# Kernel tuning notes

Hardware: AMD Instinct MI355X
Metric: run time of the kernel (lower is better)

The kernel has to match this reference:

```python
import jax, jax.numpy as jnp
import numpy as np
from jax import lax

B, C, T, L, H = 8, 32, 9, 512, 8
D = C // H  # head_dim = 4


def _l2norm(y):
    # torch F.normalize(dim=-1): x / max(||x||_2, 1e-12)
    n = jnp.sqrt(jnp.sum(y * y, axis=-1, keepdims=True))
    return y / jnp.maximum(n, 1e-12)


def setup_inputs() -> dict:
    key = jax.random.key(0)
    ks = jax.random.split(key, 12)
    def w(i, shape, s=0.05):
        return jax.random.normal(ks[i], shape, jnp.float32) * s
    return {
        "x": jax.random.normal(ks[0], (B, C, T, L), jnp.float32),
        "Wq": w(1, (C, C)), "bq": jnp.zeros((C,), jnp.float32),
        "Wk": w(2, (C, C)), "bk": jnp.zeros((C,), jnp.float32),
        "Wv": w(3, (C, C)), "bv": jnp.zeros((C,), jnp.float32),
        "Wm": w(4, (C, C)), "bm": jnp.zeros((C,), jnp.float32),
        "W_logit": jnp.eye(H, dtype=jnp.float32) + w(5, (H, H), 0.02),
        "W_ctx": jnp.eye(H, dtype=jnp.float32) + w(6, (H, H), 0.02),
        "rel_pos_bias": w(7, (H, 2 * L - 1), 0.02),
        "pre_prompt": w(8, (1, C, 1, L), 0.02),
        "conv_w": w(9, (C, C, T, 1)), "conv_b": jnp.zeros((C,), jnp.float32),
        "bn_g": jnp.ones((C,), jnp.float32), "bn_b": jnp.zeros((C,), jnp.float32),
        "pl_w": w(10, (L, L)), "pl_b": jnp.zeros((L,), jnp.float32),
        "atten_flag": 1,
    }


def _forward(x, Wq, bq, Wk, bk, Wv, bv, Wm, bm, W_logit, W_ctx,
             rel_pos_bias, pre_prompt, conv_w, conv_b, bn_g, bn_b, pl_w, pl_b):
    b = x.shape[0]
    xi = jnp.transpose(x, (0, 2, 3, 1))  # (b, t, l, c)

    def proj(W, bb):
        y = (xi @ W.T + bb).reshape(b, T, L, H, D).transpose(0, 1, 3, 2, 4)  # (b,t,h,l,d)
        return _l2norm(y)

    q = proj(Wq, bq)
    k = proj(Wk, bk)
    v = proj(Wv, bv)

    logits = jnp.einsum('bthid,bthjd->bthij', q, k) / jnp.float32(np.sqrt(D))
    idx = jnp.arange(L)
    rel = jnp.clip(idx[:, None] - idx[None, :] + (L - 1), 0, 2 * L - 2)  # (l,l)
    logits = logits + rel_pos_bias[:, rel][None, None]  # (h,l,l) broadcast over b,t
    logits = jnp.einsum('bthij,hH->btHij', logits, W_logit)
    atten = jax.nn.softmax(logits, axis=-1)
    atten = jnp.einsum('bthij,hH->btHij', atten, W_ctx)
    x_att = jnp.einsum('bthij,bthjd->bthid', atten, v)
    x_att = x_att.transpose(0, 1, 3, 2, 4).reshape(b, T, L, C)
    x_att = (x_att @ Wm.T + bm).transpose(0, 3, 1, 2)  # (b, c, t, l)

    pp = jnp.broadcast_to(pre_prompt, (b, C, 1, L))
    con = jnp.concatenate([x_att[:, :, :T - 1], pp], axis=2)  # (b, c, T, l)
    y = lax.conv_general_dilated(con, conv_w, (1, 1), 'VALID',
                                 dimension_numbers=('NCHW', 'OIHW', 'NCHW'))
    y = y + conv_b[None, :, None, None]  # (b, c, 1, l)
    # BatchNorm2d in eval with running stats (mean=0, var=1), eps=1e-5
    y = y / jnp.sqrt(jnp.float32(1.0 + 1e-5))
    y = jax.nn.relu(y * bn_g[None, :, None, None] + bn_b[None, :, None, None])
    p = y @ pl_w.T + pl_b  # Linear over last dim (token_len)
    p = x_att[:, :, T - 1:] - p
    return jnp.concatenate([x_att[:, :, :T - 1], p], axis=2)


def reference(x, Wq, bq, Wk, bk, Wv, bv, Wm, bm, W_logit, W_ctx,
              rel_pos_bias, pre_prompt, conv_w, conv_b, bn_g, bn_b,
              pl_w, pl_b, atten_flag):
    # atten_flag is accepted but unused, matching the original module
    return _forward(x, Wq, bq, Wk, bk, Wv, bv, Wm, bm, W_logit, W_ctx,
                    rel_pos_bias, pre_prompt, conv_w, conv_b, bn_g, bn_b, pl_w, pl_b)
```

## Files before the change

kernel.cpp:

```cpp
#include <hip/hip_runtime.h>
#include <math.h>

#define BB 8
#define CC 32
#define TT 9
#define LL 512
#define HH 8
#define DD 4
#define NBT (BB*TT)
#define RELN (2*LL-1)
#define RLN2 1.4426950408889634f

typedef float  f4v __attribute__((ext_vector_type(4)));
typedef int    i4v __attribute__((ext_vector_type(4)));
typedef short  s8v __attribute__((ext_vector_type(8)));

#define EXP2(x) __builtin_amdgcn_exp2f(x)

__device__ __forceinline__ unsigned cvtpk(float lo, float hi) {
  unsigned u;
  asm("v_cvt_pk_bf16_f32 %0, %1, %2" : "=v"(u) : "v"(lo), "v"(hi));
  return u;
}

__global__ __launch_bounds__(256) void prep_kernel(
    const float* __restrict__ plw, float* __restrict__ plwT,
    const float* __restrict__ rpb, const float* __restrict__ Wl,
    float* __restrict__ mbr) {
  if (blockIdx.x < 256) {
    __shared__ float tile[32][33];
    int bx = (blockIdx.x & 15) * 32, by = (blockIdx.x >> 4) * 32;
    int tx = threadIdx.x & 31, ty = threadIdx.x >> 5;
    #pragma unroll
    for (int yy = ty; yy < 32; yy += 8)
      tile[yy][tx] = plw[(by + yy)*LL + bx + tx];
    __syncthreads();
    #pragma unroll
    for (int yy = ty; yy < 32; yy += 8)
      plwT[(bx + yy)*LL + by + tx] = tile[tx][yy];
  } else {
    int x = (blockIdx.x - 256) * 256 + threadIdx.x;
    if (x >= RELN) return;
    int idx = 1022 - x;
    float r[HH];
    #pragma unroll
    for (int h = 0; h < HH; ++h) r[h] = rpb[h*RELN + idx];
    #pragma unroll
    for (int Ho = 0; Ho < HH; ++Ho) {
      float acc = 0.f;
      #pragma unroll
      for (int h = 0; h < HH; ++h) acc += r[h] * Wl[h*HH + Ho];
      mbr[Ho*1024 + x] = RLN2 * acc;
    }
  }
}

__global__ __launch_bounds__(256) void proj_kernel(
    const float* __restrict__ x,
    const float* __restrict__ Wq, const float* __restrict__ bq,
    const float* __restrict__ Wk, const float* __restrict__ bk,
    const float* __restrict__ Wv, const float* __restrict__ bv,
    float* __restrict__ qo, short* __restrict__ kbo, short* __restrict__ vt) {
  int gidx = blockIdx.x * 256 + threadIdx.x;
  int l  = gidx & (LL-1);
  int bt = gidx >> 9;
  int b = bt / TT, t = bt - b*TT;
  const int hq = blockIdx.y * 2;

  float xv[CC];
  #pragma unroll
  for (int c = 0; c < CC; ++c)
    xv[c] = x[((b*CC + c)*TT + t)*LL + l];

  #pragma unroll
  for (int h = hq; h < hq + 2; ++h) {
    float yv[DD];
    #pragma unroll
    for (int d = 0; d < DD; ++d) {
      int co = h*DD + d;
      float acc = bq[co];
      #pragma unroll
      for (int ci = 0; ci < CC; ++ci) acc += xv[ci] * Wq[co*CC + ci];
      yv[d] = acc;
    }
    float n = sqrtf(yv[0]*yv[0] + yv[1]*yv[1] + yv[2]*yv[2] + yv[3]*yv[3]);
    float inv = 0.5f * RLN2 / fmaxf(n, 1e-12f);
    *reinterpret_cast<float4*>(&qo[((size_t)bt*LL + l)*CC + h*DD]) =
        make_float4(yv[0]*inv, yv[1]*inv, yv[2]*inv, yv[3]*inv);
  }
  {
    unsigned ku[4];
    #pragma unroll
    for (int hh = 0; hh < 2; ++hh) {
      int h = hq + hh;
      float yv[DD];
      #pragma unroll
      for (int d = 0; d < DD; ++d) {
        int co = h*DD + d;
        float acc = bk[co];
        #pragma unroll
        for (int ci = 0; ci < CC; ++ci) acc += xv[ci] * Wk[co*CC + ci];
        yv[d] = acc;
      }
      float n = sqrtf(yv[0]*yv[0] + yv[1]*yv[1] + yv[2]*yv[2] + yv[3]*yv[3]);
      float inv = 1.0f / fmaxf(n, 1e-12f);
      ku[hh*2]   = cvtpk(yv[0]*inv, yv[1]*inv);
      ku[hh*2+1] = cvtpk(yv[2]*inv, yv[3]*inv);
    }
    *reinterpret_cast<uint4*>(kbo + ((size_t)bt*LL + l)*CC + hq*DD) =
        make_uint4(ku[0], ku[1], ku[2], ku[3]);
  }
  #pragma unroll
  for (int h = hq; h < hq + 2; ++h) {
    float yv[DD];
    #pragma unroll
    for (int d = 0; d < DD; ++d) {
      int co = h*DD + d;
      float acc = bv[co];
      #pragma unroll
      for (int ci = 0; ci < CC; ++ci) acc += xv[ci] * Wv[co*CC + ci];
      yv[d] = acc;
    }
    float n = sqrtf(yv[0]*yv[0] + yv[1]*yv[1] + yv[2]*yv[2] + yv[3]*yv[3]);
    float inv = 1.0f / fmaxf(n, 1e-12f);
    #pragma unroll
    for (int d = 0; d < DD; ++d) {
      unsigned u = cvtpk(yv[d]*inv, yv[d]*inv);
      int co = h*DD + d;
      reinterpret_cast<unsigned short*>(vt)[((size_t)bt*CC + co)*LL + l] =
          (unsigned short)(u & 0xffffu);
    }
  }
}

__global__ __launch_bounds__(256, 2) void attn_kernel(
    const float* __restrict__ q, const short* __restrict__ kb,
    const short* __restrict__ vt,
    const float* __restrict__ Wl, const float* __restrict__ Wc,
    const float* __restrict__ mbr,
    const float* __restrict__ Wm, const float* __restrict__ bm,
    float* __restrict__ out, float* __restrict__ xm8) {
  __shared__ float xch[2][64][9];
  __shared__ float xt[32][33];
  __shared__ float sWm[32][33];
  __shared__ float sbm[32];

  const int wgid = blockIdx.x;
  const int id   = (wgid & 7) * 144 + (wgid >> 3);
  const int bt   = id >> 4;
  const int iblk = id & 15;
  const int b    = bt / TT, t = bt - b*TT;

  const int tid  = threadIdx.x;
  const int w    = __builtin_amdgcn_readfirstlane(tid >> 6);
  const int lane = tid & 63;
  const int g    = lane >> 4;
  const int c16  = lane & 15;
  const int it   = iblk*32 + (w & 1)*16;
  const int Hb   = (w >> 1)*4;

  {
    int c4 = tid * 4;
    int co = c4 >> 5, ci = c4 & 31;
    float4 wv = *reinterpret_cast<const float4*>(Wm + co*CC + ci);
    sWm[co][ci] = wv.x; sWm[co][ci+1] = wv.y; sWm[co][ci+2] = wv.z; sWm[co][ci+3] = wv.w;
    if (tid < 32) sbm[tid] = bm[tid];
  }

  s8v bq4[4];
  {
    float qp[8];
    const float* qr = q + ((size_t)bt*LL + it + c16)*CC + g*8;
    float4 qa = *reinterpret_cast<const float4*>(qr);
    float4 qb = *reinterpret_cast<const float4*>(qr + 4);
    qp[0]=qa.x; qp[1]=qa.y; qp[2]=qa.z; qp[3]=qa.w;
    qp[4]=qb.x; qp[5]=qb.y; qp[6]=qb.z; qp[7]=qb.w;
    const int h0 = g*2;
    #pragma unroll
    for (int hh = 0; hh < 4; ++hh) {
      const int H = Hb + hh;
      const float wla = Wl[h0*HH + H];
      const float wlb = Wl[(h0+1)*HH + H];
      i4v uq;
      uq[0] = (int)cvtpk(qp[0]*wla, qp[1]*wla);
      uq[1] = (int)cvtpk(qp[2]*wla, qp[3]*wla);
      uq[2] = (int)cvtpk(qp[4]*wlb, qp[5]*wlb);
      uq[3] = (int)cvtpk(qp[6]*wlb, qp[7]*wlb);
      bq4[hh] = __builtin_bit_cast(s8v, uq);
    }
  }

  const short* kbase = kb + ((size_t)bt*LL)*CC + (size_t)c16*CC + g*8;
  const short* vb0 = vt + ((size_t)bt*CC)*LL + (size_t)c16*LL + 8*g;
  const short* vb1 = vb0 + 16*LL;
  const float* mbase = mbr + Hb*1024 + 511 + 4*g - it - c16;

  f4v t0[4], t1[4];
  float den[4];
  #pragma unroll
  for (int hh = 0; hh < 4; ++hh) {
    t0[hh] = (f4v){0.f,0.f,0.f,0.f};
    t1[hh] = (f4v){0.f,0.f,0.f,0.f};
    den[hh] = 0.f;
  }

  const int s0b = (c16 + 32*(g & 1))*4;
  const int s1b = s0b + 64;
  const bool useA = (g < 2);

  #pragma unroll 1
  for (int jp = 0; jp < 16; ++jp) {
    const int j0 = jp*32;
    s8v ak0 = *reinterpret_cast<const s8v*>(kbase + (size_t)j0*CC);
    s8v ak1 = *reinterpret_cast<const s8v*>(kbase + (size_t)(j0+16)*CC);
    s8v v0  = *reinterpret_cast<const s8v*>(vb0 + j0);
    s8v v1  = *reinterpret_cast<const s8v*>(vb1 + j0);

    #pragma unroll
    for (int hh = 0; hh < 4; ++hh) {
      const float* m = mbase + hh*1024 + j0;
      unsigned uA0, uA1, uB0, uB1;
      {
        f4v cb = { m[0], m[1], m[2], m[3] };
        f4v d = __builtin_amdgcn_mfma_f32_16x16x32_bf16(ak0, bq4[hh], cb, 0, 0, 0);
        float e0 = EXP2(d[0]), e1 = EXP2(d[1]), e2 = EXP2(d[2]), e3 = EXP2(d[3]);
        den[hh] += (e0 + e1) + (e2 + e3);
        uA0 = cvtpk(e0, e1); uA1 = cvtpk(e2, e3);
      }
      {
        f4v cb = { m[16], m[17], m[18], m[19] };
        f4v d = __builtin_amdgcn_mfma_f32_16x16x32_bf16(ak1, bq4[hh], cb, 0, 0, 0);
        float e0 = EXP2(d[0]), e1 = EXP2(d[1]), e2 = EXP2(d[2]), e3 = EXP2(d[3]);
        den[hh] += (e0 + e1) + (e2 + e3);
        uB0 = cvtpk(e0, e1); uB1 = cvtpk(e2, e3);
      }
      int a00 = __builtin_amdgcn_ds_bpermute(s0b, (int)uA0);
      int b00 = __builtin_amdgcn_ds_bpermute(s0b, (int)uB0);
      int a01 = __builtin_amdgcn_ds_bpermute(s0b, (int)uA1);
      int b01 = __builtin_amdgcn_ds_bpermute(s0b, (int)uB1);
      int a10 = __builtin_amdgcn_ds_bpermute(s1b, (int)uA0);
      int b10 = __builtin_amdgcn_ds_bpermute(s1b, (int)uB0);
      int a11 = __builtin_amdgcn_ds_bpermute(s1b, (int)uA1);
      int b11 = __builtin_amdgcn_ds_bpermute(s1b, (int)uB1);
      i4v pv;
      pv[0] = useA ? a00 : b00;
      pv[1] = useA ? a01 : b01;
      pv[2] = useA ? a10 : b10;
      pv[3] = useA ? a11 : b11;
      s8v pa = __builtin_bit_cast(s8v, pv);
      t0[hh] = __builtin_amdgcn_mfma_f32_16x16x32_bf16(pa, v0, t0[hh], 0, 0, 0);
      t1[hh] = __builtin_amdgcn_mfma_f32_16x16x32_bf16(pa, v1, t1[hh], 0, 0, 0);
    }
  }

  f4v fin0 = {0.f,0.f,0.f,0.f}, fin1 = {0.f,0.f,0.f,0.f};
  #pragma unroll
  for (int hh = 0; hh < 4; ++hh) {
    const int H = Hb + hh;
    float dn = den[hh];
    dn += __shfl_xor(dn, 16);
    dn += __shfl_xor(dn, 32);
    float inv = __builtin_amdgcn_rcpf(dn);
    const float wclo = Wc[H*HH + (c16 >> 2)];
    const float wchi = Wc[H*HH + 4 + (c16 >> 2)];
    #pragma unroll
    for (int r = 0; r < 4; ++r) {
      float ir = __int_as_float(
          __builtin_amdgcn_ds_bpermute((4*g + r)*4, __float_as_int(inv)));
      fin0[r] += t0[hh][r] * (ir * wclo);
      fin1[r] += t1[hh][r] * (ir * wchi);
    }
  }

  if (w >= 2) {
    #pragma unroll
    for (int r = 0; r < 4; ++r) {
      xch[w-2][lane][r]     = fin0[r];
      xch[w-2][lane][4 + r] = fin1[r];
    }
  }
  __syncthreads();
  if (w < 2) {
    #pragma unroll
    for (int r = 0; r < 4; ++r) {
      float o0 = fin0[r] + xch[w][lane][r];
      float o1 = fin1[r] + xch[w][lane][4 + r];
      const int row = w*16 + 4*g + r;
      xt[row][c16]      = o0;
      xt[row][16 + c16] = o1;
    }
  }
  __syncthreads();

  {
    const int row = tid & 31;
    const int cos = (tid >> 5) * 4;
    float a0 = sbm[cos], a1 = sbm[cos+1], a2 = sbm[cos+2], a3 = sbm[cos+3];
    #pragma unroll
    for (int c = 0; c < CC; ++c) {
      float xv = xt[row][c];
      a0 += xv * sWm[cos][c];
      a1 += xv * sWm[cos+1][c];
      a2 += xv * sWm[cos+2][c];
      a3 += xv * sWm[cos+3][c];
    }
    const int l = iblk*32 + row;
    float av[4] = {a0, a1, a2, a3};
    #pragma unroll
    for (int u = 0; u < 4; ++u) {
      int co = cos + u;
      if (t < TT-1) out[((b*CC + co)*TT + t)*LL + l] = av[u];
      else          xm8[(b*CC + co)*LL + l] = av[u];
    }
  }
}

__global__ __launch_bounds__(1024) void convpl_kernel(
    const float* __restrict__ out_in, const float* __restrict__ pp,
    const float* __restrict__ cw, const float* __restrict__ cb,
    const float* __restrict__ bng, const float* __restrict__ bnb,
    const float* __restrict__ plwT, const float* __restrict__ plb,
    const float* __restrict__ xm8, float* __restrict__ out) {
  __shared__ float sy[LL];
  __shared__ float part[2][LL];
  int bc = blockIdx.x;
  int b = bc >> 5, co = bc & 31;
  int tid = threadIdx.x;
  int l = tid & (LL-1);
  int h = tid >> 9;

  float acc = (h == 0) ? cb[co] : 0.f;
  #pragma unroll
  for (int cc = 0; cc < 16; ++cc) {
    int ci = h*16 + cc;
    const float* base = out_in + ((b*CC + ci)*TT)*LL + l;
    const float* wv = cw + (co*CC + ci)*TT;
    #pragma unroll
    for (int tq = 0; tq < TT-1; ++tq) acc += base[tq*LL] * wv[tq];
    acc += pp[ci*LL + l] * wv[TT-1];
  }
  part[h][l] = acc;
  __syncthreads();
  if (h == 0) {
    float scale = bng[co] * 0.999995000037499687f;
    sy[l] = fmaxf((part[0][l] + part[1][l]) * scale + bnb[co], 0.f);
  }
  __syncthreads();
  float accp = (h == 0) ? plb[l] : 0.f;
  #pragma unroll 4
  for (int lq = 0; lq < 256; ++lq) {
    int ll = h*256 + lq;
    accp += sy[ll] * plwT[ll*LL + l];
  }
  part[h][l] = accp;
  __syncthreads();
  if (h == 0)
    out[((b*CC + co)*TT + (TT-1))*LL + l] = xm8[bc*LL + l] - (part[0][l] + part[1][l]);
}

extern "C" void kernel_launch(void* const* d_in, const int* in_sizes, int n_in,
                              void* d_out, int out_size, void* d_ws, size_t ws_size,
                              hipStream_t stream) {
  const float* x    = (const float*)d_in[0];
  const float* Wq   = (const float*)d_in[1];
  const float* bq   = (const float*)d_in[2];
  const float* Wk   = (const float*)d_in[3];
  const float* bk   = (const float*)d_in[4];
  const float* Wv   = (const float*)d_in[5];
  const float* bv   = (const float*)d_in[6];
  const float* Wm   = (const float*)d_in[7];
  const float* bm   = (const float*)d_in[8];
  const float* Wl   = (const float*)d_in[9];
  const float* Wc   = (const float*)d_in[10];
  const float* rpb  = (const float*)d_in[11];
  const float* pp   = (const float*)d_in[12];
  const float* cw   = (const float*)d_in[13];
  const float* cb   = (const float*)d_in[14];
  const float* bng  = (const float*)d_in[15];
  const float* bnb  = (const float*)d_in[16];
  const float* plw  = (const float*)d_in[17];
  const float* plb  = (const float*)d_in[18];
  float* out = (float*)d_out;

  float* ws = (float*)d_ws;
  const size_t NE = (size_t)NBT*LL*CC;
  float* q_ws   = ws;
  short* kb_ws  = (short*)(q_ws + NE);
  short* vt_ws  = kb_ws + NE;
  float* xm8    = (float*)(vt_ws + NE);
  float* plwT   = xm8 + (size_t)BB*CC*LL;
  float* mbias  = plwT + (size_t)LL*LL;

  prep_kernel<<<260, 256, 0, stream>>>(plw, plwT, rpb, Wl, mbias);
  proj_kernel<<<dim3(144,4), 256, 0, stream>>>(x, Wq, bq, Wk, bk, Wv, bv,
                                               q_ws, kb_ws, vt_ws);
  attn_kernel<<<NBT*16, 256, 0, stream>>>(q_ws, kb_ws, vt_ws, Wl, Wc, mbias,
                                          Wm, bm, out, xm8);
  convpl_kernel<<<BB*CC, 1024, 0, stream>>>(out, pp, cw, cb, bng, bnb,
                                            plwT, plb, xm8, out);
}
```

Measured before the change: 108.4 us.

## Compute transposed PV product with 16x16x16 MFMA to drop bpermute shuffles

Instead of redistributing the exponentiated scores across lanes with eight ds_bpermute ops per head before a 16x16x32 MFMA, the kernel now feeds the score registers directly as the B operand of 16x16x16 bf16 MFMAs with V as the A operand. This computes the transposed output tile, so V loads become four 4-element loads and the epilogue normalisation and xt store indexing are transposed to match. The aim is to remove LDS-permute traffic and select logic from the inner loop, at the cost of twice as many (smaller) MFMA instructions issued through inline asm.

```diff
diff --git a/kernel.cpp b/kernel.cpp
--- a/kernel.cpp
+++ b/kernel.cpp
@@ -13,9 +13,14 @@
 
 typedef float  f4v __attribute__((ext_vector_type(4)));
 typedef int    i4v __attribute__((ext_vector_type(4)));
+typedef int    i2v __attribute__((ext_vector_type(2)));
 typedef short  s8v __attribute__((ext_vector_type(8)));
+typedef short  s4v __attribute__((ext_vector_type(4)));
 
 #define EXP2(x) __builtin_amdgcn_exp2f(x)
+
+#define MFMA16(acc, a, b) \
+  asm("v_mfma_f32_16x16x16_bf16 %0, %1, %2, %0" : "+v"(acc) : "v"(a), "v"(b))
 
 __device__ __forceinline__ unsigned cvtpk(float lo, float hi) {
   unsigned u;
@@ -191,7 +196,7 @@
   }
 
   const short* kbase = kb + ((size_t)bt*LL)*CC + (size_t)c16*CC + g*8;
-  const short* vb0 = vt + ((size_t)bt*CC)*LL + (size_t)c16*LL + 8*g;
+  const short* vb0 = vt + ((size_t)bt*CC)*LL + (size_t)c16*LL;
   const short* vb1 = vb0 + 16*LL;
   const float* mbase = mbr + Hb*1024 + 511 + 4*g - it - c16;
 
@@ -203,18 +208,16 @@
     t1[hh] = (f4v){0.f,0.f,0.f,0.f};
     den[hh] = 0.f;
   }
-
-  const int s0b = (c16 + 32*(g & 1))*4;
-  const int s1b = s0b + 64;
-  const bool useA = (g < 2);
 
   #pragma unroll 1
   for (int jp = 0; jp < 16; ++jp) {
     const int j0 = jp*32;
     s8v ak0 = *reinterpret_cast<const s8v*>(kbase + (size_t)j0*CC);
     s8v ak1 = *reinterpret_cast<const s8v*>(kbase + (size_t)(j0+16)*CC);
-    s8v v0  = *reinterpret_cast<const s8v*>(vb0 + j0);
-    s8v v1  = *reinterpret_cast<const s8v*>(vb1 + j0);
+    s4v va00 = *reinterpret_cast<const s4v*>(vb0 + j0 + 4*g);
+    s4v va01 = *reinterpret_cast<const s4v*>(vb0 + j0 + 16 + 4*g);
+    s4v va10 = *reinterpret_cast<const s4v*>(vb1 + j0 + 4*g);
+    s4v va11 = *reinterpret_cast<const s4v*>(vb1 + j0 + 16 + 4*g);
 
     #pragma unroll
     for (int hh = 0; hh < 4; ++hh) {
@@ -224,32 +227,22 @@
         f4v cb = { m[0], m[1], m[2], m[3] };
         f4v d = __builtin_amdgcn_mfma_f32_16x16x32_bf16(ak0, bq4[hh], cb, 0, 0, 0);
         float e0 = EXP2(d[0]), e1 = EXP2(d[1]), e2 = EXP2(d[2]), e3 = EXP2(d[3]);
+        uA0 = cvtpk(e0, e1); uA1 = cvtpk(e2, e3);
         den[hh] += (e0 + e1) + (e2 + e3);
-        uA0 = cvtpk(e0, e1); uA1 = cvtpk(e2, e3);
       }
       {
         f4v cb = { m[16], m[17], m[18], m[19] };
         f4v d = __builtin_amdgcn_mfma_f32_16x16x32_bf16(ak1, bq4[hh], cb, 0, 0, 0);
         float e0 = EXP2(d[0]), e1 = EXP2(d[1]), e2 = EXP2(d[2]), e3 = EXP2(d[3]);
+        uB0 = cvtpk(e0, e1); uB1 = cvtpk(e2, e3);
         den[hh] += (e0 + e1) + (e2 + e3);
-        uB0 = cvtpk(e0, e1); uB1 = cvtpk(e2, e3);
       }
-      int a00 = __builtin_amdgcn_ds_bpermute(s0b, (int)uA0);
-      int b00 = __builtin_amdgcn_ds_bpermute(s0b, (int)uB0);
-      int a01 = __builtin_amdgcn_ds_bpermute(s0b, (int)uA1);
-      int b01 = __builtin_amdgcn_ds_bpermute(s0b, (int)uB1);
-      int a10 = __builtin_amdgcn_ds_bpermute(s1b, (int)uA0);
-      int b10 = __builtin_amdgcn_ds_bpermute(s1b, (int)uB0);
-      int a11 = __builtin_amdgcn_ds_bpermute(s1b, (int)uA1);
-      int b11 = __builtin_amdgcn_ds_bpermute(s1b, (int)uB1);
-      i4v pv;
-      pv[0] = useA ? a00 : b00;
-      pv[1] = useA ? a01 : b01;
-      pv[2] = useA ? a10 : b10;
-      pv[3] = useA ? a11 : b11;
-      s8v pa = __builtin_bit_cast(s8v, pv);
-      t0[hh] = __builtin_amdgcn_mfma_f32_16x16x32_bf16(pa, v0, t0[hh], 0, 0, 0);
-      t1[hh] = __builtin_amdgcn_mfma_f32_16x16x32_bf16(pa, v1, t1[hh], 0, 0, 0);
+      s4v pA = __builtin_bit_cast(s4v, (i2v){(int)uA0, (int)uA1});
+      s4v pB = __builtin_bit_cast(s4v, (i2v){(int)uB0, (int)uB1});
+      MFMA16(t0[hh], va00, pA);
+      MFMA16(t1[hh], va10, pA);
+      MFMA16(t0[hh], va01, pB);
+      MFMA16(t1[hh], va11, pB);
     }
   }
 
@@ -261,14 +254,12 @@
     dn += __shfl_xor(dn, 16);
     dn += __shfl_xor(dn, 32);
     float inv = __builtin_amdgcn_rcpf(dn);
-    const float wclo = Wc[H*HH + (c16 >> 2)];
-    const float wchi = Wc[H*HH + 4 + (c16 >> 2)];
+    const float slo = inv * Wc[H*HH + g];
+    const float shi = inv * Wc[H*HH + 4 + g];
     #pragma unroll
     for (int r = 0; r < 4; ++r) {
-      float ir = __int_as_float(
-          __builtin_amdgcn_ds_bpermute((4*g + r)*4, __float_as_int(inv)));
-      fin0[r] += t0[hh][r] * (ir * wclo);
-      fin1[r] += t1[hh][r] * (ir * wchi);
+      fin0[r] += t0[hh][r] * slo;
+      fin1[r] += t1[hh][r] * shi;
     }
   }
 
@@ -285,9 +276,9 @@
     for (int r = 0; r < 4; ++r) {
       float o0 = fin0[r] + xch[w][lane][r];
       float o1 = fin1[r] + xch[w][lane][4 + r];
-      const int row = w*16 + 4*g + r;
-      xt[row][c16]      = o0;
-      xt[row][16 + c16] = o1;
+      const int row = w*16 + c16;
+      xt[row][4*g + r]      = o0;
+      xt[row][16 + 4*g + r] = o1;
     }
   }
   __syncthreads();
```

Result: slower. 120.8 us (+11.4%).

## Merge prep and projection kernels, stage bias in LDS, restructure conv kernel

Applied to the files above, without the earlier changes.

Folds the weight-transpose/bias-precompute kernel into the projection kernel as extra blocks, removing one launch. In the attention kernel the per-head relative bias window is copied into shared memory once per block instead of read from global memory each iteration. The conv/linear tail kernel now handles two (b,co) rows per 1024-thread block with full reductions per thread, instead of splitting each reduction across halves, which halves the block count and drops one barrier and partial sum. This adds about 17KB of LDS per attention block, which may reduce occupancy, and doubles per-thread serial work in the tail kernel.

```diff
diff --git a/kernel.cpp b/kernel.cpp
--- a/kernel.cpp
+++ b/kernel.cpp
@@ -10,6 +10,7 @@
 #define NBT (BB*TT)
 #define RELN (2*LL-1)
 #define RLN2 1.4426950408889634f
+#define SMBW 544
 
 typedef float  f4v __attribute__((ext_vector_type(4)));
 typedef int    i4v __attribute__((ext_vector_type(4)));
@@ -23,49 +24,52 @@
   return u;
 }
 
-__global__ __launch_bounds__(256) void prep_kernel(
-    const float* __restrict__ plw, float* __restrict__ plwT,
-    const float* __restrict__ rpb, const float* __restrict__ Wl,
-    float* __restrict__ mbr) {
-  if (blockIdx.x < 256) {
-    __shared__ float tile[32][33];
-    int bx = (blockIdx.x & 15) * 32, by = (blockIdx.x >> 4) * 32;
-    int tx = threadIdx.x & 31, ty = threadIdx.x >> 5;
-    #pragma unroll
-    for (int yy = ty; yy < 32; yy += 8)
-      tile[yy][tx] = plw[(by + yy)*LL + bx + tx];
-    __syncthreads();
-    #pragma unroll
-    for (int yy = ty; yy < 32; yy += 8)
-      plwT[(bx + yy)*LL + by + tx] = tile[tx][yy];
-  } else {
-    int x = (blockIdx.x - 256) * 256 + threadIdx.x;
-    if (x >= RELN) return;
-    int idx = 1022 - x;
-    float r[HH];
-    #pragma unroll
-    for (int h = 0; h < HH; ++h) r[h] = rpb[h*RELN + idx];
-    #pragma unroll
-    for (int Ho = 0; Ho < HH; ++Ho) {
-      float acc = 0.f;
-      #pragma unroll
-      for (int h = 0; h < HH; ++h) acc += r[h] * Wl[h*HH + Ho];
-      mbr[Ho*1024 + x] = RLN2 * acc;
-    }
-  }
-}
-
-__global__ __launch_bounds__(256) void proj_kernel(
+__global__ __launch_bounds__(256) void pre_kernel(
     const float* __restrict__ x,
     const float* __restrict__ Wq, const float* __restrict__ bq,
     const float* __restrict__ Wk, const float* __restrict__ bk,
     const float* __restrict__ Wv, const float* __restrict__ bv,
-    float* __restrict__ qo, short* __restrict__ kbo, short* __restrict__ vt) {
-  int gidx = blockIdx.x * 256 + threadIdx.x;
+    float* __restrict__ qo, short* __restrict__ kbo, short* __restrict__ vt,
+    const float* __restrict__ plw, float* __restrict__ plwT,
+    const float* __restrict__ rpb, const float* __restrict__ Wl,
+    float* __restrict__ mbr) {
+  __shared__ float tile[32][33];
+  if (blockIdx.x >= 576) {
+    int pid = blockIdx.x - 576;
+    if (pid < 256) {
+      int bx = (pid & 15) * 32, by = (pid >> 4) * 32;
+      int tx = threadIdx.x & 31, ty = threadIdx.x >> 5;
+      #pragma unroll
+      for (int yy = ty; yy < 32; yy += 8)
+        tile[yy][tx] = plw[(by + yy)*LL + bx + tx];
+      __syncthreads();
+      #pragma unroll
+      for (int yy = ty; yy < 32; yy += 8)
+        plwT[(bx + yy)*LL + by + tx] = tile[tx][yy];
+    } else {
+      int xx = (pid - 256) * 256 + threadIdx.x;
+      if (xx >= RELN) return;
+      int idx = 1022 - xx;
+      float r[HH];
+      #pragma unroll
+      for (int h = 0; h < HH; ++h) r[h] = rpb[h*RELN + idx];
+      #pragma unroll
+      for (int Ho = 0; Ho < HH; ++Ho) {
+        float acc = 0.f;
+        #pragma unroll
+        for (int h = 0; h < HH; ++h) acc += r[h] * Wl[h*HH + Ho];
+        mbr[Ho*1024 + xx] = RLN2 * acc;
+      }
+    }
+    return;
+  }
+
+  int bid = blockIdx.x;
+  int gidx = (bid % 144) * 256 + threadIdx.x;
   int l  = gidx & (LL-1);
   int bt = gidx >> 9;
   int b = bt / TT, t = bt - b*TT;
-  const int hq = blockIdx.y * 2;
+  const int hq = (bid / 144) * 2;
 
   float xv[CC];
   #pragma unroll
@@ -140,6 +144,7 @@
     const float* __restrict__ mbr,
     const float* __restrict__ Wm, const float* __restrict__ bm,
     float* __restrict__ out, float* __restrict__ xm8) {
+  __shared__ float smb[HH][SMBW];
   __shared__ float xch[2][64][9];
   __shared__ float xt[32][33];
   __shared__ float sWm[32][33];
@@ -159,6 +164,13 @@
   const int it   = iblk*32 + (w & 1)*16;
   const int Hb   = (w >> 1)*4;
 
+  {
+    const int xbase = 480 - 32*iblk;
+    for (int s = tid; s < HH*SMBW; s += 256) {
+      int h = s / SMBW, sx = s - h*SMBW;
+      smb[h][sx] = mbr[h*1024 + xbase + sx];
+    }
+  }
   {
     int c4 = tid * 4;
     int co = c4 >> 5, ci = c4 & 31;
@@ -189,11 +201,12 @@
       bq4[hh] = __builtin_bit_cast(s8v, uq);
     }
   }
+  __syncthreads();
 
   const short* kbase = kb + ((size_t)bt*LL)*CC + (size_t)c16*CC + g*8;
   const short* vb0 = vt + ((size_t)bt*CC)*LL + (size_t)c16*LL + 8*g;
   const short* vb1 = vb0 + 16*LL;
-  const float* mbase = mbr + Hb*1024 + 511 + 4*g - it - c16;
+  const int sx0 = 31 + 4*g - 16*(w & 1) - c16;
 
   f4v t0[4], t1[4];
   float den[4];
@@ -218,7 +231,7 @@
 
     #pragma unroll
     for (int hh = 0; hh < 4; ++hh) {
-      const float* m = mbase + hh*1024 + j0;
+      const float* m = &smb[Hb + hh][sx0 + j0];
       unsigned uA0, uA1, uB0, uB1;
       {
         f4v cb = { m[0], m[1], m[2], m[3] };
@@ -321,41 +334,32 @@
     const float* __restrict__ bng, const float* __restrict__ bnb,
     const float* __restrict__ plwT, const float* __restrict__ plb,
     const float* __restrict__ xm8, float* __restrict__ out) {
-  __shared__ float sy[LL];
-  __shared__ float part[2][LL];
-  int bc = blockIdx.x;
-  int b = bc >> 5, co = bc & 31;
+  __shared__ float sy[2][LL];
+  int bc0 = blockIdx.x * 2;
   int tid = threadIdx.x;
   int l = tid & (LL-1);
-  int h = tid >> 9;
-
-  float acc = (h == 0) ? cb[co] : 0.f;
-  #pragma unroll
-  for (int cc = 0; cc < 16; ++cc) {
-    int ci = h*16 + cc;
+  int p = tid >> 9;
+  int bc = bc0 + p;
+  int b = bc >> 5, co = bc & 31;
+
+  float acc = cb[co];
+  #pragma unroll
+  for (int ci = 0; ci < CC; ++ci) {
     const float* base = out_in + ((b*CC + ci)*TT)*LL + l;
     const float* wv = cw + (co*CC + ci)*TT;
     #pragma unroll
     for (int tq = 0; tq < TT-1; ++tq) acc += base[tq*LL] * wv[tq];
     acc += pp[ci*LL + l] * wv[TT-1];
   }
-  part[h][l] = acc;
+  float scale = bng[co] * 0.999995000037499687f;
+  sy[p][l] = fmaxf(acc * scale + bnb[co], 0.f);
   __syncthreads();
-  if (h == 0) {
-    float scale = bng[co] * 0.999995000037499687f;
-    sy[l] = fmaxf((part[0][l] + part[1][l]) * scale + bnb[co], 0.f);
-  }
-  __syncthreads();
-  float accp = (h == 0) ? plb[l] : 0.f;
+
+  float accp = plb[l];
   #pragma unroll 4
-  for (int lq = 0; lq < 256; ++lq) {
-    int ll = h*256 + lq;
-    accp += sy[ll] * plwT[ll*LL + l];
-  }
-  part[h][l] = accp;
-  __syncthreads();
-  if (h == 0)
-    out[((b*CC + co)*TT + (TT-1))*LL + l] = xm8[bc*LL + l] - (part[0][l] + part[1][l]);
+  for (int ll = 0; ll < LL; ++ll)
+    accp += sy[p][ll] * plwT[ll*LL + l];
+  out[((b*CC + co)*TT + (TT-1))*LL + l] = xm8[bc*LL + l] - accp;
 }
 
 extern "C" void kernel_launch(void* const* d_in, const int* in_sizes, int n_in,
@@ -391,11 +395,11 @@
   float* plwT   = xm8 + (size_t)BB*CC*LL;
   float* mbias  = plwT + (size_t)LL*LL;
 
-  prep_kernel<<<260, 256, 0, stream>>>(plw, plwT, rpb, Wl, mbias);
-  proj_kernel<<<dim3(144,4), 256, 0, stream>>>(x, Wq, bq, Wk, bk, Wv, bv,
-                                               q_ws, kb_ws, vt_ws);
+  pre_kernel<<<836, 256, 0, stream>>>(x, Wq, bq, Wk, bk, Wv, bv,
+                                      q_ws, kb_ws, vt_ws,
+                                      plw, plwT, rpb, Wl, mbias);
   attn_kernel<<<NBT*16, 256, 0, stream>>>(q_ws, kb_ws, vt_ws, Wl, Wc, mbias,
                                           Wm, bm, out, xm8);
-  convpl_kernel<<<BB*CC, 1024, 0, stream>>>(out, pp, cw, cb, bng, bnb,
-                                            plwT, plb, xm8, out);
+  convpl_kernel<<<128, 1024, 0, stream>>>(out, pp, cw, cb, bng, bnb,
+                                          plwT, plb, xm8, out);
 }
```

New measurement: 125.3 us. 1.16x slower.
